# Performance work log

Measured on AMD Instinct MI355X. Metric: run time of the kernel, lower is better.

The kernel has to match this reference:

```python
import jax, jax.numpy as jnp
import numpy as np

N_NODES = 50000
N_RELS = 8
IN_DIM = 128
OUT_DIM = 128
N_EDGES = 800000


def setup_inputs() -> dict:
    key = jax.random.key(0)
    k1, k2, k3, k4 = jax.random.split(key, 4)
    src = jax.random.randint(k1, (N_EDGES,), 0, N_NODES, dtype=jnp.int64 if jax.config.jax_enable_x64 else jnp.int32)
    rel = jax.random.randint(k2, (N_EDGES,), 0, N_RELS, dtype=src.dtype)
    tgt = jax.random.randint(k3, (N_EDGES,), 0, N_NODES, dtype=src.dtype)
    triples = jnp.stack([src, rel, tgt], axis=1)  # (E, 3) like torch layout (s, r, t)
    features = jax.random.normal(k4, (N_NODES, IN_DIM), dtype=jnp.float32)
    weights = jax.random.normal(jax.random.fold_in(key, 1), (N_RELS, IN_DIM, OUT_DIM), dtype=jnp.float32) * (1.0 / np.sqrt(IN_DIM))
    bias = jnp.zeros((OUT_DIM,), dtype=jnp.float32)
    return {"triples": triples, "features": features, "weights": weights, "bias": bias}


def reference(triples, features, weights, bias):
    # RGCN-NC forward, horizontal stacking (featured mode):
    #   out[t] = sum_{(s,r,t) in E} (1/c_{t,r}) * features[s] @ W[r] + bias
    # where c_{t,r} = #edges sharing the same (relation, target) pair,
    # matching sum_sparse(..., row_normalisation=False) on the (n x r*n) adjacency.
    src, rel, tgt = triples[:, 0], triples[:, 1], triples[:, 2]
    n = features.shape[0]
    r = weights.shape[0]
    e = triples.shape[0]

    # per-(rel, tgt) edge counts -> 1/c normalization per edge
    key = rel * n + tgt  # column index of horizontally stacked adjacency
    counts = jax.ops.segment_sum(jnp.ones((e,), dtype=features.dtype), key, num_segments=r * n)
    vals = 1.0 / counts[key]  # (E,)

    # dense per-relation transform: H[r] = X @ W[r]   (r, n, out)
    h = jnp.einsum('ni,rio->rno', features, weights)

    # gather per-edge messages, scale, scatter-add into targets
    msgs = h[rel, src] * vals[:, None]  # (E, out)
    out = jax.ops.segment_sum(msgs, tgt, num_segments=n)  # (n, out)
    return out + bias
```

## Files before the change

kernel.cpp:

```cpp
#include <hip/hip_runtime.h>
#include <hip/hip_bf16.h>

#define N_NODES 50000
#define N_RELS 8
#define IN_DIM 128
#define OUT_DIM 128
#define N_EDGES 800000
#define NR (N_NODES * N_RELS)
#define KDIM (N_RELS * IN_DIM)
#define SCAN_ELEMS 2048
#define SCAN_NBLK ((NR + SCAN_ELEMS - 1) / SCAN_ELEMS)
#define FUSE_BLKS 1563
#define CNT_BLKS ((N_EDGES / 4 + 255) / 256)
#define CW_BLKS ((N_RELS * IN_DIM * OUT_DIM + 255) / 256)
#define FB_BLKS ((N_NODES * IN_DIM / 8 + 255) / 256)

typedef __attribute__((ext_vector_type(8))) short bf16x8;
typedef __attribute__((ext_vector_type(4))) float floatx4;
typedef __attribute__((ext_vector_type(4))) unsigned int uintx4;

__device__ inline unsigned short f2bf(float f) {
    unsigned u = __builtin_bit_cast(unsigned, f);
    u += 0x7fff + ((u >> 16) & 1);
    return (unsigned short)(u >> 16);
}
__device__ inline float bflo(unsigned u) {
    return __builtin_bit_cast(float, u << 16);
}
__device__ inline float bfhi(unsigned u) {
    return __builtin_bit_cast(float, u & 0xffff0000u);
}

__global__ void prep_kernel(const int* __restrict__ tri, const float* __restrict__ W,
                            const float* __restrict__ features,
                            int* __restrict__ cnt, unsigned short* __restrict__ Wtf,
                            unsigned short* __restrict__ featB) {
    const int b = blockIdx.x;
    if (b < CNT_BLKS) {
        int t = b * 256 + threadIdx.x;
        if (t >= N_EDGES / 4) return;
        const int4* tri4 = (const int4*)tri;
        int4 a = tri4[3 * t], v = tri4[3 * t + 1], c = tri4[3 * t + 2];
        atomicAdd(&cnt[a.z * N_RELS + a.y], 1);
        atomicAdd(&cnt[v.y * N_RELS + v.x], 1);
        atomicAdd(&cnt[c.x * N_RELS + v.w], 1);
        atomicAdd(&cnt[c.w * N_RELS + c.z], 1);
    } else if (b < CNT_BLKS + CW_BLKS) {
        int idx = (b - CNT_BLKS) * 256 + threadIdx.x;
        if (idx >= N_RELS * IN_DIM * OUT_DIM) return;
        int e  = idx & 7;
        int l  = (idx >> 3) & 63;
        int ks = (idx >> 9) & 31;
        int nt = idx >> 14;
        int o = nt * 16 + (l & 15);
        int k = ks * 32 + (l >> 4) * 8 + e;
        Wtf[idx] = f2bf(W[(k >> 7) * (IN_DIM * OUT_DIM) + (k & 127) * OUT_DIM + o]);
    } else {
        int t = (b - CNT_BLKS - CW_BLKS) * 256 + threadIdx.x;
        if (t >= N_NODES * IN_DIM / 8) return;
        const float4* f4 = (const float4*)features;
        float4 x = f4[2 * t], y = f4[2 * t + 1];
        uint4 o;
        o.x = (unsigned)f2bf(x.x) | ((unsigned)f2bf(x.y) << 16);
        o.y = (unsigned)f2bf(x.z) | ((unsigned)f2bf(x.w) << 16);
        o.z = (unsigned)f2bf(y.x) | ((unsigned)f2bf(y.y) << 16);
        o.w = (unsigned)f2bf(y.z) | ((unsigned)f2bf(y.w) << 16);
        ((uint4*)featB)[t] = o;
    }
}

__global__ void scan_part(const int* __restrict__ cnt, int* __restrict__ bsum) {
    __shared__ int s[256];
    int b = blockIdx.x, t = threadIdx.x;
    int base = b * SCAN_ELEMS + t * 8;
    int sum = 0;
#pragma unroll
    for (int k = 0; k < 8; ++k) {
        int i = base + k;
        sum += (i < NR) ? cnt[i] : 0;
    }
    s[t] = sum; __syncthreads();
    for (int off = 128; off > 0; off >>= 1) {
        if (t < off) s[t] += s[t + off];
        __syncthreads();
    }
    if (t == 0) bsum[b] = s[0];
}

__global__ __launch_bounds__(256) void scan_fused(
    const int* __restrict__ cnt, const int* __restrict__ bsum,
    int* __restrict__ segOff, int* __restrict__ cursor)
{
    __shared__ int s[256];
    __shared__ int sboff;
    const int b = blockIdx.x, t = threadIdx.x;

    int vb = (t < SCAN_NBLK) ? bsum[t] : 0;
    s[t] = vb; __syncthreads();
    for (int off = 1; off < 256; off <<= 1) {
        int x = (t >= off) ? s[t - off] : 0;
        __syncthreads();
        s[t] += x;
        __syncthreads();
    }
    if (t == 0) sboff = (b == 0) ? 0 : s[b - 1];
    __syncthreads();
    const int boff = sboff;

    const int base = b * SCAN_ELEMS + t * 8;
    int v[8]; int sum = 0;
#pragma unroll
    for (int k = 0; k < 8; ++k) {
        int i = base + k;
        v[k] = (i < NR) ? cnt[i] : 0;
        sum += v[k];
    }
    s[t] = sum; __syncthreads();
    for (int off = 1; off < 256; off <<= 1) {
        int x = (t >= off) ? s[t - off] : 0;
        __syncthreads();
        s[t] += x;
        __syncthreads();
    }
    int run = boff + s[t] - sum;
#pragma unroll
    for (int k = 0; k < 8; ++k) {
        int i = base + k;
        if (i < NR) { segOff[i] = run; cursor[i] = run; run += v[k]; }
    }
    if (b == 0 && t == 0) segOff[NR] = N_EDGES;
}

__global__ void scatter_kernel(const int* __restrict__ tri, int* __restrict__ cursor,
                               int* __restrict__ sortedSrc) {
    int e = blockIdx.x * 256 + threadIdx.x;
    if (e >= N_EDGES) return;
    int src = tri[3 * e];
    int rel = tri[3 * e + 1];
    int tgt = tri[3 * e + 2];
    int p = atomicAdd(&cursor[tgt * N_RELS + rel], 1);
    sortedSrc[p] = src;
}

__global__ __launch_bounds__(512, 8) void fused_kernel(
    const int* __restrict__ sortedSrc, const int* __restrict__ segOff,
    const unsigned short* __restrict__ featB,
    const unsigned short* __restrict__ Wtf,
    const float* __restrict__ bias,
    float* __restrict__ out)
{
    __shared__ unsigned short Atile[32 * 512];
    const int tid = threadIdx.x;
    const int wave = tid >> 6, lane = tid & 63;
    const int q = lane >> 4, l16 = lane & 15;
    const int m0 = blockIdx.x * 32;
    const int wm = wave & 1, wn = wave >> 1;

    floatx4 acc[2];
#pragma unroll
    for (int nt = 0; nt < 2; ++nt) acc[nt] = (floatx4){0.f, 0.f, 0.f, 0.f};

    const unsigned short* fb = featB + 8 * l16;

#pragma unroll
    for (int p = 0; p < 2; ++p) {
        for (int i = 0; i < 4; ++i) {
            const int nl = wave * 4 + i;
            const int node = m0 + nl;
            if (node < N_NODES) {
                int bnd = 0;
                if (lane < 5) bnd = segOff[node * N_RELS + 4 * p + lane];
                int sg[5];
#pragma unroll
                for (int k = 0; k < 5; ++k) sg[k] = __shfl(bnd, k);

                const int e0 = sg[0], eN = sg[4];
                int srcw = 0;
                if (e0 + lane < eN) srcw = sortedSrc[e0 + lane];

                const int s0v = sg[q], s1v = sg[q + 1];
                const int len = s1v - s0v;
                int m0x = __shfl_xor(len, 16);
                int jm = (len > m0x) ? len : m0x;
                int m1x = __shfl_xor(jm, 32);
                const int jmax = (jm > m1x) ? jm : m1x;
                float a0 = 0.f, a1 = 0.f, a2 = 0.f, a3 = 0.f;
                float a4 = 0.f, a5 = 0.f, a6 = 0.f, a7 = 0.f;
                for (int j = 0; j < jmax; j += 2) {
                    const int ea = s0v + j;
                    const int ia = ea - e0;
                    const int swina = __shfl(srcw, ia & 63);
                    const int ib = ia + 1;
                    const int swinb = __shfl(srcw, ib & 63);
                    const bool pa = j < len;
                    const bool pb = j + 1 < len;
                    int srca = 0, srcb = 0;
                    if (pa) srca = (ia < 64) ? swina : sortedSrc[ea];
                    if (pb) srcb = (ib < 64) ? swinb : sortedSrc[ea + 1];
                    uint4 ua = *(const uint4*)&fb[srca * IN_DIM];
                    uint4 ub = *(const uint4*)&fb[srcb * IN_DIM];
                    if (pa) {
                        a0 += bflo(ua.x); a1 += bfhi(ua.x);
                        a2 += bflo(ua.y); a3 += bfhi(ua.y);
                        a4 += bflo(ua.z); a5 += bfhi(ua.z);
                        a6 += bflo(ua.w); a7 += bfhi(ua.w);
                    }
                    if (pb) {
                        a0 += bflo(ub.x); a1 += bfhi(ub.x);
                        a2 += bflo(ub.y); a3 += bfhi(ub.y);
                        a4 += bflo(ub.z); a5 += bfhi(ub.z);
                        a6 += bflo(ub.w); a7 += bfhi(ub.w);
                    }
                }
                const float inv = (len > 0) ? 1.0f / (float)len : 0.0f;
                uintx4 pk;
                pk[0] = (unsigned)f2bf(a0 * inv) | ((unsigned)f2bf(a1 * inv) << 16);
                pk[1] = (unsigned)f2bf(a2 * inv) | ((unsigned)f2bf(a3 * inv) << 16);
                pk[2] = (unsigned)f2bf(a4 * inv) | ((unsigned)f2bf(a5 * inv) << 16);
                pk[3] = (unsigned)f2bf(a6 * inv) | ((unsigned)f2bf(a7 * inv) << 16);
                const int us = (q * 16 + l16) ^ (nl & 15);
                *(uintx4*)&Atile[(nl * 64 + us) * 8] = pk;
            }
        }
        __syncthreads();

#pragma unroll
        for (int ksl = 0; ksl < 16; ++ksl) {
            const int ks = p * 16 + ksl;
            const int r = wm * 16 + l16;
            const int us = (ksl * 4 + q) ^ (r & 15);
            bf16x8 a = *(const bf16x8*)&Atile[(r * 64 + us) * 8];
#pragma unroll
            for (int nt = 0; nt < 2; ++nt) {
                const int ntg = wn * 2 + nt;
                bf16x8 b = *(const bf16x8*)&Wtf[(size_t)((ntg * 32 + ks) * 64 + lane) * 8];
                acc[nt] = __builtin_amdgcn_mfma_f32_16x16x32_bf16(a, b, acc[nt], 0, 0, 0);
            }
        }
        __syncthreads();
    }

#pragma unroll
    for (int nt = 0; nt < 2; ++nt) {
        const int o = (wn * 2 + nt) * 16 + l16;
        const float bv = bias[o];
#pragma unroll
        for (int j = 0; j < 4; ++j) {
            const int t = m0 + wm * 16 + q * 4 + j;
            if (t < N_NODES)
                __builtin_nontemporal_store(acc[nt][j] + bv,
                                            &out[(size_t)t * OUT_DIM + o]);
        }
    }
}

extern "C" void kernel_launch(void* const* d_in, const int* in_sizes, int n_in,
                              void* d_out, int out_size, void* d_ws, size_t ws_size,
                              hipStream_t stream)
{
    const int*   tri      = (const int*)d_in[0];
    const float* features = (const float*)d_in[1];
    const float* W        = (const float*)d_in[2];
    const float* bias     = (const float*)d_in[3];
    float* out = (float*)d_out;

    char* ws = (char*)d_ws;
    unsigned short* Wtf = (unsigned short*)ws; ws += (size_t)OUT_DIM * KDIM * 2;
    int* cnt       = (int*)ws; ws += (size_t)NR * 4;
    int* segOff    = (int*)ws; ws += (size_t)(NR + 4) * 4;
    int* cursor    = (int*)ws; ws += (size_t)NR * 4;
    int* bsum      = (int*)ws; ws += (size_t)SCAN_NBLK * 4;
    int* sortedSrc = (int*)ws; ws += (size_t)N_EDGES * 4;
    unsigned short* featB = (unsigned short*)ws; ws += (size_t)N_NODES * IN_DIM * 2;
    (void)ws_size; (void)in_sizes; (void)n_in; (void)out_size;

    hipMemsetAsync(cnt, 0, NR * sizeof(int), stream);
    prep_kernel<<<CNT_BLKS + CW_BLKS + FB_BLKS, 256, 0, stream>>>(tri, W, features, cnt, Wtf, featB);
    scan_part<<<SCAN_NBLK, 256, 0, stream>>>(cnt, bsum);
    scan_fused<<<SCAN_NBLK, 256, 0, stream>>>(cnt, bsum, segOff, cursor);
    scatter_kernel<<<(N_EDGES + 255) / 256, 256, 0, stream>>>(tri, cursor, sortedSrc);
    fused_kernel<<<FUSE_BLKS, 512, 0, stream>>>(sortedSrc, segOff, featB, Wtf, bias, out);
}
```

Baseline: 249.1 us.

## Vectorize scatter loads, stage output through LDS, raise MFMA wave priority

The scatter kernel now has each thread handle four edges, reading the triples with three int4 loads instead of twelve scalar loads, and launches a quarter as many blocks. The fused kernel's epilogue writes accumulators into shared memory and then emits coalesced 16-byte nontemporal row stores, replacing scattered scalar stores. s_setprio is raised around the MFMA loop to favour waves doing matrix math. The cost is an extra barrier and an LDS round-trip in the epilogue, and less parallelism in the scatter kernel.

Result: slower. 256.5 us (+3.0%).

```diff
diff --git a/kernel.cpp b/kernel.cpp
--- a/kernel.cpp
+++ b/kernel.cpp
@@ -133,13 +133,18 @@
 
 __global__ void scatter_kernel(const int* __restrict__ tri, int* __restrict__ cursor,
                                int* __restrict__ sortedSrc) {
-    int e = blockIdx.x * 256 + threadIdx.x;
-    if (e >= N_EDGES) return;
-    int src = tri[3 * e];
-    int rel = tri[3 * e + 1];
-    int tgt = tri[3 * e + 2];
-    int p = atomicAdd(&cursor[tgt * N_RELS + rel], 1);
-    sortedSrc[p] = src;
+    int t = blockIdx.x * 256 + threadIdx.x;
+    if (t >= N_EDGES / 4) return;
+    const int4* tri4 = (const int4*)tri;
+    int4 a = tri4[3 * t], v = tri4[3 * t + 1], c = tri4[3 * t + 2];
+    int p0 = atomicAdd(&cursor[a.z * N_RELS + a.y], 1);
+    int p1 = atomicAdd(&cursor[v.y * N_RELS + v.x], 1);
+    int p2 = atomicAdd(&cursor[c.x * N_RELS + v.w], 1);
+    int p3 = atomicAdd(&cursor[c.w * N_RELS + c.z], 1);
+    sortedSrc[p0] = a.x;
+    sortedSrc[p1] = a.w;
+    sortedSrc[p2] = v.z;
+    sortedSrc[p3] = c.y;
 }
 
 __global__ __launch_bounds__(512, 8) void fused_kernel(
@@ -149,7 +154,7 @@
     const float* __restrict__ bias,
     float* __restrict__ out)
 {
-    __shared__ unsigned short Atile[32 * 512];
+    __shared__ __align__(16) unsigned short Atile[32 * 512];
     const int tid = threadIdx.x;
     const int wave = tid >> 6, lane = tid & 63;
     const int q = lane >> 4, l16 = lane & 15;
@@ -224,6 +229,7 @@
         }
         __syncthreads();
 
+        __builtin_amdgcn_s_setprio(1);
 #pragma unroll
         for (int ksl = 0; ksl < 16; ++ksl) {
             const int ks = p * 16 + ksl;
@@ -237,19 +243,32 @@
                 acc[nt] = __builtin_amdgcn_mfma_f32_16x16x32_bf16(a, b, acc[nt], 0, 0, 0);
             }
         }
-        __syncthreads();
-    }
-
+        __builtin_amdgcn_s_setprio(0);
+        __syncthreads();
+    }
+
+    float* fbuf = (float*)Atile;
 #pragma unroll
     for (int nt = 0; nt < 2; ++nt) {
         const int o = (wn * 2 + nt) * 16 + l16;
         const float bv = bias[o];
 #pragma unroll
         for (int j = 0; j < 4; ++j) {
-            const int t = m0 + wm * 16 + q * 4 + j;
-            if (t < N_NODES)
-                __builtin_nontemporal_store(acc[nt][j] + bv,
-                                            &out[(size_t)t * OUT_DIM + o]);
+            const int r = wm * 16 + q * 4 + j;
+            fbuf[r * 128 + o] = acc[nt][j] + bv;
+        }
+    }
+    __syncthreads();
+    {
+        const int row = tid >> 4;
+        const int col = (tid & 15) * 8;
+        const int node = m0 + row;
+        if (node < N_NODES) {
+            floatx4 w0 = *(const floatx4*)&fbuf[row * 128 + col];
+            floatx4 w1 = *(const floatx4*)&fbuf[row * 128 + col + 4];
+            float* po = &out[(size_t)node * OUT_DIM + col];
+            __builtin_nontemporal_store(w0, (floatx4*)po);
+            __builtin_nontemporal_store(w1, (floatx4*)(po + 4));
         }
     }
 }
@@ -278,6 +297,6 @@
     prep_kernel<<<CNT_BLKS + CW_BLKS + FB_BLKS, 256, 0, stream>>>(tri, W, features, cnt, Wtf, featB);
     scan_part<<<SCAN_NBLK, 256, 0, stream>>>(cnt, bsum);
     scan_fused<<<SCAN_NBLK, 256, 0, stream>>>(cnt, bsum, segOff, cursor);
-    scatter_kernel<<<(N_EDGES + 255) / 256, 256, 0, stream>>>(tri, cursor, sortedSrc);
+    scatter_kernel<<<CNT_BLKS, 256, 0, stream>>>(tri, cursor, sortedSrc);
     fused_kernel<<<FUSE_BLKS, 512, 0, stream>>>(sortedSrc, segOff, featB, Wtf, bias, out);
 }
```
